# Kernel tuning notes

Hardware: AMD Instinct MI355X
Metric: run time of the kernel (lower is better)

Reference implementation:

```python
import jax, jax.numpy as jnp
import numpy as np

BLOCK = 32           # sparsity_config.block
STRIDE_BLOCKS = 4    # stride 128 // block 32
B, H, L, HD = 2, 16, 4096, 64


def _make_fixed_layout(nb, bs):
    """DeepSpeed 'fixed' unidirectional layout, numverts=vertsize=1 (same for all heads)."""
    lay = np.zeros((nb, nb), dtype=np.int64)
    # local: lower-triangular within each stride window
    for i in range(0, nb, bs):
        for j in range(i, i + bs):
            lay[j, i:j + 1] = 1
    # global: vertical stripe at column offset bs-1 of every window, causal (col < row)
    start = bs - 1
    for i in range(nb):
        for j in range(start, i, bs):
            lay[i, j] = 1
    rows, cols = np.nonzero(lay)  # sorted by row
    return jnp.asarray(rows, jnp.int32), jnp.asarray(cols, jnp.int32)


def setup_inputs() -> dict:
    key = jax.random.key(0)
    kq, kk, kv = jax.random.split(key, 3)
    query = jax.random.normal(kq, (B, H, L, HD), jnp.float32)
    key_t = jax.random.normal(kk, (B, H, L, HD), jnp.float32)
    value = jax.random.normal(kv, (B, H, L, HD), jnp.float32)
    rows, cols = _make_fixed_layout(L // BLOCK, STRIDE_BLOCKS)
    return {"query": query, "key": key_t, "value": value,
            "rows": rows, "cols": cols, "block": BLOCK}


def reference(query, key, value, rows, cols, block):
    b, h, l, hd = query.shape
    nb = l // block
    scale = float(hd) ** (-0.5)
    # [nb, B, H, block, hd] with block-row axis leading for gather/scatter
    qb = jnp.moveaxis(query.reshape(b, h, nb, block, hd), 2, 0)
    kb = jnp.moveaxis(key.reshape(b, h, nb, block, hd), 2, 0)
    vb = jnp.moveaxis(value.reshape(b, h, nb, block, hd), 2, 0)
    # sdd: scores only on active blocks -> [nnz, B, H, block, block]
    s = jnp.einsum('nbhqd,nbhkd->nbhqk', qb[rows], kb[cols]) * scale
    # block-sparse softmax over each query row (segment reduce over blocks sharing a row)
    m_blk = s.max(-1)  # [nnz, B, H, block]
    row_max = jnp.full((nb, b, h, block), -jnp.inf, s.dtype).at[rows].max(m_blk)
    e = jnp.exp(s - row_max[rows][..., None])
    denom = jnp.zeros((nb, b, h, block), s.dtype).at[rows].add(e.sum(-1))
    p = e / denom[rows][..., None]
    # dsd: probs @ value, scatter-add into block rows
    ob = jnp.zeros((nb, b, h, block, hd), s.dtype).at[rows].add(
        jnp.einsum('nbhqk,nbhkd->nbhqd', p, vb[cols]))
    return jnp.moveaxis(ob, 0, 2).reshape(b, h, l, hd)
```

## Files before the change

### kernel.cpp

```cpp
#include <hip/hip_runtime.h>
#include <math.h>

#define BH    32
#define LSEQ  4096
#define HD    64
#define BLK   32
#define NB    128
#define NWIN  32
#define QSCALE 0.18033688011112042f

#define KSTR 34
#define VSTR 17

typedef _Float16 h2  __attribute__((ext_vector_type(2)));
typedef _Float16 h8  __attribute__((ext_vector_type(8)));
typedef float    f16v __attribute__((ext_vector_type(16)));

static __device__ __forceinline__ h2 pk(float a, float b) {
    return __builtin_bit_cast(h2, __builtin_amdgcn_cvt_pkrtz(a, b));
}
static __device__ __forceinline__ unsigned pku(float a, float b) {
    return __builtin_bit_cast(unsigned, __builtin_amdgcn_cvt_pkrtz(a, b));
}
static __device__ __forceinline__ short h16(float x) {
    return __builtin_bit_cast(short, (_Float16)x);
}
static __device__ __forceinline__ h8 mk8(h2 a, h2 b, h2 c, h2 d) {
    h8 r;
    r[0] = a[0]; r[1] = a[1]; r[2] = b[0]; r[3] = b[1];
    r[4] = c[0]; r[5] = c[1]; r[6] = d[0]; r[7] = d[1];
    return r;
}

__global__ __launch_bounds__(256)
void sparse_attn_pair(const float* __restrict__ Q, const float* __restrict__ K,
                      const float* __restrict__ V, float* __restrict__ out)
{
    const int id = (int)blockIdx.x;
    const int bh = id & 31;
    const int p  = id >> 5;

    const int t    = (int)threadIdx.x;
    const int d    = t >> 6;
    const int lane = t & 63;
    const int l31  = lane & 31;
    const int h    = lane >> 5;

    __shared__ __align__(16) unsigned kbuf[2][BLK * KSTR];
    __shared__ __align__(16) unsigned vbuf[2][HD * VSTR];

    const size_t base = (size_t)bh * (LSEQ * HD);

    const int srow = t >> 3;
    const int sdg  = t & 7;

    const float* kgb = K + base + (size_t)srow * HD + sdg * 8;
    const float* vgb = V + base + (size_t)srow * HD + sdg * 8;

    float4 kA, kB, vA, vB;

    auto loadR = [&](int w, int j) {
        const int col = (j < w) ? (4 * j + 3) : (4 * w + (j - w));
        const size_t off = (size_t)col * (BLK * HD);
        kA = *(const float4*)(kgb + off);
        kB = *(const float4*)(kgb + off + 4);
        vA = *(const float4*)(vgb + off);
        vB = *(const float4*)(vgb + off + 4);
    };
    auto writeL = [&](int b) {
        uint2 w0, w1;
        w0.x = pku(kA.x, kA.y); w0.y = pku(kA.z, kA.w);
        w1.x = pku(kB.x, kB.y); w1.y = pku(kB.z, kB.w);
        *(uint2*)&kbuf[b][srow * KSTR + sdg * 4]     = w0;
        *(uint2*)&kbuf[b][srow * KSTR + sdg * 4 + 2] = w1;
        short* vs = (short*)&vbuf[b][0];
        const int vd0 = sdg * 8;
        vs[(vd0 + 0) * (2 * VSTR) + srow] = h16(vA.x);
        vs[(vd0 + 1) * (2 * VSTR) + srow] = h16(vA.y);
        vs[(vd0 + 2) * (2 * VSTR) + srow] = h16(vA.z);
        vs[(vd0 + 3) * (2 * VSTR) + srow] = h16(vA.w);
        vs[(vd0 + 4) * (2 * VSTR) + srow] = h16(vB.x);
        vs[(vd0 + 5) * (2 * VSTR) + srow] = h16(vB.y);
        vs[(vd0 + 6) * (2 * VSTR) + srow] = h16(vB.z);
        vs[(vd0 + 7) * (2 * VSTR) + srow] = h16(vB.w);
    };

    int pb = 0;
    loadR(p, 0);

    for (int ph = 0; ph < 2; ++ph) {
        const int w = ph ? (31 - p) : p;
        const int r = 4 * w + d;
        const int n = w + 4;

        const float* qp = Q + base + (size_t)(r * BLK + l31) * HD + 8 * h;
        h8 qf[4];
#pragma unroll
        for (int tt = 0; tt < 4; ++tt) {
            float4 a = *(const float4*)(qp + 16 * tt);
            float4 b = *(const float4*)(qp + 16 * tt + 4);
            qf[tt] = mk8(pk(a.x * QSCALE, a.y * QSCALE), pk(a.z * QSCALE, a.w * QSCALE),
                         pk(b.x * QSCALE, b.y * QSCALE), pk(b.z * QSCALE, b.w * QSCALE));
        }

        f16v o0 = {}, o1 = {};
        float2 ls2 = make_float2(0.0f, 0.0f);

        for (int j = 0; j < n; ++j, pb ^= 1) {
            writeL(pb);
            if (j + 1 < n)      loadR(w, j + 1);
            else if (ph == 0)   loadR(31 - p, 0);
            __builtin_amdgcn_s_waitcnt(0xc07f);
            __builtin_amdgcn_s_barrier();

            if (j < w || (j - w) <= d) {
                const unsigned* kb = kbuf[pb];
                const unsigned* vb = vbuf[pb];

                f16v st = {};
#pragma unroll
                for (int tt = 0; tt < 4; ++tt) {
                    const int kw = l31 * KSTR + 8 * tt + 4 * h;
                    uint2 u0 = *(const uint2*)&kb[kw];
                    uint2 u1 = *(const uint2*)&kb[kw + 2];
                    uint4 uu; uu.x = u0.x; uu.y = u0.y; uu.z = u1.x; uu.w = u1.y;
                    h8 kf = __builtin_bit_cast(h8, uu);
                    st = __builtin_amdgcn_mfma_f32_32x32x16_f16(kf, qf[tt], st, 0, 0, 0);
                }

                float ps[16];
#pragma unroll
                for (int g = 0; g < 16; ++g) ps[g] = __builtin_exp2f(st[g]);
#pragma unroll
                for (int g = 0; g < 8; ++g) {
                    ls2.x += ps[2 * g];
                    ls2.y += ps[2 * g + 1];
                }
                h2 ph2[8];
#pragma unroll
                for (int jj = 0; jj < 8; ++jj) ph2[jj] = pk(ps[2 * jj], ps[2 * jj + 1]);

#pragma unroll
                for (int t2 = 0; t2 < 2; ++t2) {
                    h2 s0 = h ? ph2[4 * t2]     : ph2[4 * t2 + 2];
                    h2 s1 = h ? ph2[4 * t2 + 1] : ph2[4 * t2 + 3];
                    int i0 = __shfl_xor(__builtin_bit_cast(int, s0), 32);
                    int i1 = __shfl_xor(__builtin_bit_cast(int, s1), 32);
                    h2 g0 = __builtin_bit_cast(h2, i0), g1 = __builtin_bit_cast(h2, i1);
                    h2 c0 = h ? g0 : ph2[4 * t2];
                    h2 c1 = h ? g1 : ph2[4 * t2 + 1];
                    h2 c2 = h ? ph2[4 * t2 + 2] : g0;
                    h2 c3 = h ? ph2[4 * t2 + 3] : g1;
                    h8 pa = mk8(c0, c1, c2, c3);

                    const int va0 = l31 * VSTR + 8 * t2 + 4 * h;
                    const int va1 = (32 + l31) * VSTR + 8 * t2 + 4 * h;
                    uint4 u0, u1;
                    u0.x = vb[va0]; u0.y = vb[va0 + 1]; u0.z = vb[va0 + 2]; u0.w = vb[va0 + 3];
                    u1.x = vb[va1]; u1.y = vb[va1 + 1]; u1.z = vb[va1 + 2]; u1.w = vb[va1 + 3];
                    h8 vf0 = __builtin_bit_cast(h8, u0);
                    h8 vf1 = __builtin_bit_cast(h8, u1);
                    o0 = __builtin_amdgcn_mfma_f32_32x32x16_f16(pa, vf0, o0, 0, 0, 0);
                    o1 = __builtin_amdgcn_mfma_f32_32x32x16_f16(pa, vf1, o1, 0, 0, 0);
                }
            }
        }

        float lsum = ls2.x + ls2.y;
        lsum += __shfl_xor(lsum, 32);
        const float inv = 1.0f / lsum;

        float* op = out + base + (size_t)(r * BLK) * HD;
#pragma unroll
        for (int g = 0; g < 16; ++g) {
            const int qrow = (g & 3) + 8 * (g >> 2) + 4 * h;
            int iv = __builtin_amdgcn_ds_bpermute(qrow << 2, __float_as_int(inv));
            const float invq = __int_as_float(iv);
            op[(size_t)qrow * HD + l31]      = o0[g] * invq;
            op[(size_t)qrow * HD + 32 + l31] = o1[g] * invq;
        }
    }
}

extern "C" void kernel_launch(void* const* d_in, const int* in_sizes, int n_in,
                              void* d_out, int out_size, void* d_ws, size_t ws_size,
                              hipStream_t stream) {
    const float* Q = (const float*)d_in[0];
    const float* K = (const float*)d_in[1];
    const float* V = (const float*)d_in[2];

    dim3 grid(NWIN * BH / 2);
    dim3 block(256);
    sparse_attn_pair<<<grid, block, 0, stream>>>(Q, K, V, (float*)d_out);
}
```

Measured before the change: 165.5 us.

## Assign one window per block with two query row-blocks per wave

Replaces the paired-window, 4-wave blocks with one window per 128-thread block, where each wave handles two query row-blocks and shares the K fragment loads and V fragment loads between them. The grid doubles to 1024 blocks, and blocks are ordered so that neighbouring blocks receive balanced window lengths across heads. The ordering is meant to spread load evenly over CUs and to reuse LDS reads across two MFMA chains. In exchange, each thread holds more registers (two Q fragment sets and four accumulators), staging per thread doubles, and the barrier becomes raw inline asm.

```diff
diff --git a/kernel.cpp b/kernel.cpp
--- a/kernel.cpp
+++ b/kernel.cpp
@@ -12,6 +12,8 @@
 #define KSTR 34
 #define VSTR 17
 
+#define RAW_BARRIER() asm volatile("s_waitcnt lgkmcnt(0)\n\ts_barrier" ::: "memory")
+
 typedef _Float16 h2  __attribute__((ext_vector_type(2)));
 typedef _Float16 h8  __attribute__((ext_vector_type(8)));
 typedef float    f16v __attribute__((ext_vector_type(16)));
@@ -32,154 +34,201 @@
     return r;
 }
 
-__global__ __launch_bounds__(256)
-void sparse_attn_pair(const float* __restrict__ Q, const float* __restrict__ K,
-                      const float* __restrict__ V, float* __restrict__ out)
+__global__ __launch_bounds__(128)
+void sparse_attn_r2f(const float* __restrict__ Q, const float* __restrict__ K,
+                     const float* __restrict__ V, float* __restrict__ out)
 {
     const int id = (int)blockIdx.x;
-    const int bh = id & 31;
-    const int p  = id >> 5;
+    const int cc = id & 255;
+    const int kk = id >> 8;
+    const int v  = cc & 31;
+    const int u  = cc >> 5;
+    const int bh = u + 8 * kk;
+    int w;
+    switch (kk) {
+        case 0:  w = v;              break;
+        case 1:  w = (47 - v) & 31;  break;
+        case 2:  w = (v + 16) & 31;  break;
+        default: w = (63 - v) & 31;  break;
+    }
 
     const int t    = (int)threadIdx.x;
-    const int d    = t >> 6;
+    const int wid  = t >> 6;
     const int lane = t & 63;
     const int l31  = lane & 31;
     const int h    = lane >> 5;
+    const int d0   = 2 * wid, d1 = 2 * wid + 1;
+    const int r0   = 4 * w + d0, r1 = r0 + 1;
 
     __shared__ __align__(16) unsigned kbuf[2][BLK * KSTR];
     __shared__ __align__(16) unsigned vbuf[2][HD * VSTR];
 
     const size_t base = (size_t)bh * (LSEQ * HD);
 
-    const int srow = t >> 3;
-    const int sdg  = t & 7;
-
-    const float* kgb = K + base + (size_t)srow * HD + sdg * 8;
-    const float* vgb = V + base + (size_t)srow * HD + sdg * 8;
-
-    float4 kA, kB, vA, vB;
-
-    auto loadR = [&](int w, int j) {
+    h8 qf0[4], qf1[4];
+    {
+        const float* qp0 = Q + base + (size_t)(r0 * BLK + l31) * HD + 8 * h;
+        const float* qp1 = Q + base + (size_t)(r1 * BLK + l31) * HD + 8 * h;
+#pragma unroll
+        for (int tt = 0; tt < 4; ++tt) {
+            float4 a = *(const float4*)(qp0 + 16 * tt);
+            float4 b = *(const float4*)(qp0 + 16 * tt + 4);
+            qf0[tt] = mk8(pk(a.x * QSCALE, a.y * QSCALE), pk(a.z * QSCALE, a.w * QSCALE),
+                          pk(b.x * QSCALE, b.y * QSCALE), pk(b.z * QSCALE, b.w * QSCALE));
+            float4 c = *(const float4*)(qp1 + 16 * tt);
+            float4 e = *(const float4*)(qp1 + 16 * tt + 4);
+            qf1[tt] = mk8(pk(c.x * QSCALE, c.y * QSCALE), pk(c.z * QSCALE, c.w * QSCALE),
+                          pk(e.x * QSCALE, e.y * QSCALE), pk(e.z * QSCALE, e.w * QSCALE));
+        }
+    }
+
+    f16v o00 = {}, o01 = {}, o10 = {}, o11 = {};
+    float2 ls0 = make_float2(0.0f, 0.0f);
+    float2 ls1 = make_float2(0.0f, 0.0f);
+
+    const int n    = w + 4;
+    const int srow = t >> 2;
+    const int sdg  = t & 3;
+
+    const float* kgb = K + base + (size_t)srow * HD + sdg * 16;
+    const float* vgb = V + base + (size_t)srow * HD + sdg * 16;
+
+    float4 kq0, kq1, kq2, kq3, vq0, vq1, vq2, vq3;
+
+    auto loadR = [&](int j) {
         const int col = (j < w) ? (4 * j + 3) : (4 * w + (j - w));
         const size_t off = (size_t)col * (BLK * HD);
-        kA = *(const float4*)(kgb + off);
-        kB = *(const float4*)(kgb + off + 4);
-        vA = *(const float4*)(vgb + off);
-        vB = *(const float4*)(vgb + off + 4);
+        kq0 = *(const float4*)(kgb + off);
+        kq1 = *(const float4*)(kgb + off + 4);
+        kq2 = *(const float4*)(kgb + off + 8);
+        kq3 = *(const float4*)(kgb + off + 12);
+        vq0 = *(const float4*)(vgb + off);
+        vq1 = *(const float4*)(vgb + off + 4);
+        vq2 = *(const float4*)(vgb + off + 8);
+        vq3 = *(const float4*)(vgb + off + 12);
     };
     auto writeL = [&](int b) {
-        uint2 w0, w1;
-        w0.x = pku(kA.x, kA.y); w0.y = pku(kA.z, kA.w);
-        w1.x = pku(kB.x, kB.y); w1.y = pku(kB.z, kB.w);
-        *(uint2*)&kbuf[b][srow * KSTR + sdg * 4]     = w0;
-        *(uint2*)&kbuf[b][srow * KSTR + sdg * 4 + 2] = w1;
+        unsigned* kb = &kbuf[b][srow * KSTR + sdg * 8];
+        uint2 w0, w1, w2, w3;
+        w0.x = pku(kq0.x, kq0.y); w0.y = pku(kq0.z, kq0.w);
+        w1.x = pku(kq1.x, kq1.y); w1.y = pku(kq1.z, kq1.w);
+        w2.x = pku(kq2.x, kq2.y); w2.y = pku(kq2.z, kq2.w);
+        w3.x = pku(kq3.x, kq3.y); w3.y = pku(kq3.z, kq3.w);
+        *(uint2*)&kb[0] = w0;
+        *(uint2*)&kb[2] = w1;
+        *(uint2*)&kb[4] = w2;
+        *(uint2*)&kb[6] = w3;
         short* vs = (short*)&vbuf[b][0];
-        const int vd0 = sdg * 8;
-        vs[(vd0 + 0) * (2 * VSTR) + srow] = h16(vA.x);
-        vs[(vd0 + 1) * (2 * VSTR) + srow] = h16(vA.y);
-        vs[(vd0 + 2) * (2 * VSTR) + srow] = h16(vA.z);
-        vs[(vd0 + 3) * (2 * VSTR) + srow] = h16(vA.w);
-        vs[(vd0 + 4) * (2 * VSTR) + srow] = h16(vB.x);
-        vs[(vd0 + 5) * (2 * VSTR) + srow] = h16(vB.y);
-        vs[(vd0 + 6) * (2 * VSTR) + srow] = h16(vB.z);
-        vs[(vd0 + 7) * (2 * VSTR) + srow] = h16(vB.w);
-    };
-
+        const int vd0 = sdg * 16;
+        vs[(vd0 +  0) * (2 * VSTR) + srow] = h16(vq0.x);
+        vs[(vd0 +  1) * (2 * VSTR) + srow] = h16(vq0.y);
+        vs[(vd0 +  2) * (2 * VSTR) + srow] = h16(vq0.z);
+        vs[(vd0 +  3) * (2 * VSTR) + srow] = h16(vq0.w);
+        vs[(vd0 +  4) * (2 * VSTR) + srow] = h16(vq1.x);
+        vs[(vd0 +  5) * (2 * VSTR) + srow] = h16(vq1.y);
+        vs[(vd0 +  6) * (2 * VSTR) + srow] = h16(vq1.z);
+        vs[(vd0 +  7) * (2 * VSTR) + srow] = h16(vq1.w);
+        vs[(vd0 +  8) * (2 * VSTR) + srow] = h16(vq2.x);
+        vs[(vd0 +  9) * (2 * VSTR) + srow] = h16(vq2.y);
+        vs[(vd0 + 10) * (2 * VSTR) + srow] = h16(vq2.z);
+        vs[(vd0 + 11) * (2 * VSTR) + srow] = h16(vq2.w);
+        vs[(vd0 + 12) * (2 * VSTR) + srow] = h16(vq3.x);
+        vs[(vd0 + 13) * (2 * VSTR) + srow] = h16(vq3.y);
+        vs[(vd0 + 14) * (2 * VSTR) + srow] = h16(vq3.z);
+        vs[(vd0 + 15) * (2 * VSTR) + srow] = h16(vq3.w);
+    };
+
+    auto smpv = [&](const f16v& st, float2& ls, f16v& oa, f16v& ob,
+                    const h8& vf00, const h8& vf01,
+                    const h8& vf10, const h8& vf11) {
+        float ps[16];
+#pragma unroll
+        for (int g = 0; g < 16; ++g) ps[g] = __builtin_exp2f(st[g]);
+#pragma unroll
+        for (int g = 0; g < 8; ++g) {
+            ls.x += ps[2 * g];
+            ls.y += ps[2 * g + 1];
+        }
+        h2 ph2[8];
+#pragma unroll
+        for (int jj = 0; jj < 8; ++jj) ph2[jj] = pk(ps[2 * jj], ps[2 * jj + 1]);
+#pragma unroll
+        for (int t2 = 0; t2 < 2; ++t2) {
+            h2 s0 = h ? ph2[4 * t2]     : ph2[4 * t2 + 2];
+            h2 s1 = h ? ph2[4 * t2 + 1] : ph2[4 * t2 + 3];
+            int i0 = __shfl_xor(__builtin_bit_cast(int, s0), 32);
+            int i1 = __shfl_xor(__builtin_bit_cast(int, s1), 32);
+            h2 g0 = __builtin_bit_cast(h2, i0), g1 = __builtin_bit_cast(h2, i1);
+            h2 c0 = h ? g0 : ph2[4 * t2];
+            h2 c1 = h ? g1 : ph2[4 * t2 + 1];
+            h2 c2 = h ? ph2[4 * t2 + 2] : g0;
+            h2 c3 = h ? ph2[4 * t2 + 3] : g1;
+            h8 pa = mk8(c0, c1, c2, c3);
+            oa = __builtin_amdgcn_mfma_f32_32x32x16_f16(pa, t2 ? vf10 : vf00, oa, 0, 0, 0);
+            ob = __builtin_amdgcn_mfma_f32_32x32x16_f16(pa, t2 ? vf11 : vf01, ob, 0, 0, 0);
+        }
+    };
+
+    loadR(0);
     int pb = 0;
-    loadR(p, 0);
-
-    for (int ph = 0; ph < 2; ++ph) {
-        const int w = ph ? (31 - p) : p;
-        const int r = 4 * w + d;
-        const int n = w + 4;
-
-        const float* qp = Q + base + (size_t)(r * BLK + l31) * HD + 8 * h;
-        h8 qf[4];
-#pragma unroll
-        for (int tt = 0; tt < 4; ++tt) {
-            float4 a = *(const float4*)(qp + 16 * tt);
-            float4 b = *(const float4*)(qp + 16 * tt + 4);
-            qf[tt] = mk8(pk(a.x * QSCALE, a.y * QSCALE), pk(a.z * QSCALE, a.w * QSCALE),
-                         pk(b.x * QSCALE, b.y * QSCALE), pk(b.z * QSCALE, b.w * QSCALE));
-        }
-
-        f16v o0 = {}, o1 = {};
-        float2 ls2 = make_float2(0.0f, 0.0f);
-
-        for (int j = 0; j < n; ++j, pb ^= 1) {
-            writeL(pb);
-            if (j + 1 < n)      loadR(w, j + 1);
-            else if (ph == 0)   loadR(31 - p, 0);
-            __builtin_amdgcn_s_waitcnt(0xc07f);
-            __builtin_amdgcn_s_barrier();
-
-            if (j < w || (j - w) <= d) {
-                const unsigned* kb = kbuf[pb];
-                const unsigned* vb = vbuf[pb];
-
-                f16v st = {};
-#pragma unroll
-                for (int tt = 0; tt < 4; ++tt) {
-                    const int kw = l31 * KSTR + 8 * tt + 4 * h;
-                    uint2 u0 = *(const uint2*)&kb[kw];
-                    uint2 u1 = *(const uint2*)&kb[kw + 2];
-                    uint4 uu; uu.x = u0.x; uu.y = u0.y; uu.z = u1.x; uu.w = u1.y;
-                    h8 kf = __builtin_bit_cast(h8, uu);
-                    st = __builtin_amdgcn_mfma_f32_32x32x16_f16(kf, qf[tt], st, 0, 0, 0);
-                }
-
-                float ps[16];
-#pragma unroll
-                for (int g = 0; g < 16; ++g) ps[g] = __builtin_exp2f(st[g]);
-#pragma unroll
-                for (int g = 0; g < 8; ++g) {
-                    ls2.x += ps[2 * g];
-                    ls2.y += ps[2 * g + 1];
-                }
-                h2 ph2[8];
-#pragma unroll
-                for (int jj = 0; jj < 8; ++jj) ph2[jj] = pk(ps[2 * jj], ps[2 * jj + 1]);
-
-#pragma unroll
-                for (int t2 = 0; t2 < 2; ++t2) {
-                    h2 s0 = h ? ph2[4 * t2]     : ph2[4 * t2 + 2];
-                    h2 s1 = h ? ph2[4 * t2 + 1] : ph2[4 * t2 + 3];
-                    int i0 = __shfl_xor(__builtin_bit_cast(int, s0), 32);
-                    int i1 = __shfl_xor(__builtin_bit_cast(int, s1), 32);
-                    h2 g0 = __builtin_bit_cast(h2, i0), g1 = __builtin_bit_cast(h2, i1);
-                    h2 c0 = h ? g0 : ph2[4 * t2];
-                    h2 c1 = h ? g1 : ph2[4 * t2 + 1];
-                    h2 c2 = h ? ph2[4 * t2 + 2] : g0;
-                    h2 c3 = h ? ph2[4 * t2 + 3] : g1;
-                    h8 pa = mk8(c0, c1, c2, c3);
-
-                    const int va0 = l31 * VSTR + 8 * t2 + 4 * h;
-                    const int va1 = (32 + l31) * VSTR + 8 * t2 + 4 * h;
-                    uint4 u0, u1;
-                    u0.x = vb[va0]; u0.y = vb[va0 + 1]; u0.z = vb[va0 + 2]; u0.w = vb[va0 + 3];
-                    u1.x = vb[va1]; u1.y = vb[va1 + 1]; u1.z = vb[va1 + 2]; u1.w = vb[va1 + 3];
-                    h8 vf0 = __builtin_bit_cast(h8, u0);
-                    h8 vf1 = __builtin_bit_cast(h8, u1);
-                    o0 = __builtin_amdgcn_mfma_f32_32x32x16_f16(pa, vf0, o0, 0, 0, 0);
-                    o1 = __builtin_amdgcn_mfma_f32_32x32x16_f16(pa, vf1, o1, 0, 0, 0);
-                }
+
+    for (int j = 0; j < n; ++j, pb ^= 1) {
+        writeL(pb);
+        if (j + 1 < n) loadR(j + 1);
+        RAW_BARRIER();
+
+        const int jj = j - w;
+        const bool act1 = (jj < 0) || (jj <= d1);
+        const bool act0 = (jj < 0) || (jj <= d0);
+        if (act1) {
+            const unsigned* kb = kbuf[pb];
+            const unsigned* vb = vbuf[pb];
+
+            f16v st0 = {}, st1 = {};
+#pragma unroll
+            for (int tt = 0; tt < 4; ++tt) {
+                const int kw = l31 * KSTR + 8 * tt + 4 * h;
+                uint2 u0 = *(const uint2*)&kb[kw];
+                uint2 u1 = *(const uint2*)&kb[kw + 2];
+                uint4 uu; uu.x = u0.x; uu.y = u0.y; uu.z = u1.x; uu.w = u1.y;
+                h8 kf = __builtin_bit_cast(h8, uu);
+                st1 = __builtin_amdgcn_mfma_f32_32x32x16_f16(kf, qf1[tt], st1, 0, 0, 0);
+                st0 = __builtin_amdgcn_mfma_f32_32x32x16_f16(kf, qf0[tt], st0, 0, 0, 0);
             }
-        }
-
-        float lsum = ls2.x + ls2.y;
+
+            const int va = l31 * VSTR + 4 * h;
+            const int vc = (32 + l31) * VSTR + 4 * h;
+            uint4 x00, x01, x10, x11;
+            x00.x = vb[va];     x00.y = vb[va + 1];  x00.z = vb[va + 2];  x00.w = vb[va + 3];
+            x01.x = vb[vc];     x01.y = vb[vc + 1];  x01.z = vb[vc + 2];  x01.w = vb[vc + 3];
+            x10.x = vb[va + 8]; x10.y = vb[va + 9];  x10.z = vb[va + 10]; x10.w = vb[va + 11];
+            x11.x = vb[vc + 8]; x11.y = vb[vc + 9];  x11.z = vb[vc + 10]; x11.w = vb[vc + 11];
+            h8 vf00 = __builtin_bit_cast(h8, x00);
+            h8 vf01 = __builtin_bit_cast(h8, x01);
+            h8 vf10 = __builtin_bit_cast(h8, x10);
+            h8 vf11 = __builtin_bit_cast(h8, x11);
+
+            smpv(st1, ls1, o10, o11, vf00, vf01, vf10, vf11);
+            if (act0) smpv(st0, ls0, o00, o01, vf00, vf01, vf10, vf11);
+        }
+    }
+
+    auto finish = [&](float2 ls, const f16v& oa, const f16v& ob, int r) {
+        float lsum = ls.x + ls.y;
         lsum += __shfl_xor(lsum, 32);
         const float inv = 1.0f / lsum;
-
         float* op = out + base + (size_t)(r * BLK) * HD;
 #pragma unroll
         for (int g = 0; g < 16; ++g) {
             const int qrow = (g & 3) + 8 * (g >> 2) + 4 * h;
             int iv = __builtin_amdgcn_ds_bpermute(qrow << 2, __float_as_int(inv));
             const float invq = __int_as_float(iv);
-            op[(size_t)qrow * HD + l31]      = o0[g] * invq;
-            op[(size_t)qrow * HD + 32 + l31] = o1[g] * invq;
-        }
-    }
+            op[(size_t)qrow * HD + l31]      = oa[g] * invq;
+            op[(size_t)qrow * HD + 32 + l31] = ob[g] * invq;
+        }
+    };
+    finish(ls0, o00, o01, r0);
+    finish(ls1, o10, o11, r1);
 }
 
 extern "C" void kernel_launch(void* const* d_in, const int* in_sizes, int n_in,
@@ -189,7 +238,7 @@
     const float* K = (const float*)d_in[1];
     const float* V = (const float*)d_in[2];
 
-    dim3 grid(NWIN * BH / 2);
-    dim3 block(256);
-    sparse_attn_pair<<<grid, block, 0, stream>>>(Q, K, V, (float*)d_out);
-}
+    dim3 grid(NWIN * BH);
+    dim3 block(128);
+    sparse_attn_r2f<<<grid, block, 0, stream>>>(Q, K, V, (float*)d_out);
+}
```

Measured after the change: 173.7 us. +5.0%, slower.
